# Kernel tuning notes

Measured on AMD Instinct MI355X. Metric: run time of the kernel, lower is better.

Reference implementation:

```python
import jax, jax.numpy as jnp
import numpy as np
import math

B, S, D = 2, 2048, 1024
H = 16
HD = D // H
FFN = 2048
E = 8
TOP_K = 2
CAP_FACTOR = 1.25
EPS = 1e-6
BASE = 10000.0
CAP = max(math.ceil(B * S * TOP_K * CAP_FACTOR / E), 1)  # 1280


def setup_inputs() -> dict:
    key = jax.random.key(0)
    ks = jax.random.split(key, 6)
    sd = 0.02
    return {
        "x": jax.random.normal(ks[0], (B, S, D), jnp.float32),
        "g1": jnp.ones((D,), jnp.float32),
        "w_qkv": jax.random.normal(ks[1], (D, 3 * D), jnp.float32) * sd,
        "w_o": jax.random.normal(ks[2], (D, D), jnp.float32) * sd,
        "g2": jnp.ones((D,), jnp.float32),
        "w_router": jax.random.normal(ks[3], (D, E), jnp.float32) * sd,
        "w1": jax.random.normal(ks[4], (E, D, FFN), jnp.float32) * sd,
        "w2": jax.random.normal(ks[5], (E, FFN, D), jnp.float32) * sd,
    }


def _rmsnorm(x, w):
    rms = jax.lax.rsqrt(jnp.mean(x * x, axis=-1, keepdims=True) + EPS)
    return w * x * rms


def _rope(x, cos, sin):
    # x: [b,h,s,hd]; consecutive pairs (2i, 2i+1) form complex numbers
    xr = x[..., 0::2]
    xi = x[..., 1::2]
    c = cos[None, None]  # [1,1,s,hd/2]
    s_ = sin[None, None]
    out_r = xr * c - xi * s_
    out_i = xr * s_ + xi * c
    return jnp.stack([out_r, out_i], axis=-1).reshape(x.shape)


def _mha(x, w_qkv, w_o):
    b, s, d = x.shape
    qkv = x @ w_qkv
    q, k, v = jnp.split(qkv, 3, axis=-1)
    to_heads = lambda z: z.reshape(b, s, H, HD).transpose(0, 2, 1, 3)
    q, k, v = to_heads(q), to_heads(k), to_heads(v)
    # rotary embedding
    theta = BASE ** (-2.0 * (jnp.arange(HD // 2, dtype=jnp.float32) / HD))
    freqs = jnp.arange(s, dtype=jnp.float32)[:, None] * theta[None, :]  # [s,hd/2]
    cos, sin = jnp.cos(freqs), jnp.sin(freqs)
    q = _rope(q, cos, sin)
    k = _rope(k, cos, sin)
    scores = jnp.einsum('bhqd,bhkd->bhqk', q, k) / jnp.sqrt(jnp.float32(HD))
    causal = jnp.tril(jnp.ones((s, s), dtype=bool))
    scores = jnp.where(causal, scores, -jnp.inf)
    attn = jax.nn.softmax(scores, axis=-1)
    y = jnp.einsum('bhqk,bhkd->bhqd', attn, v)
    y = y.transpose(0, 2, 1, 3).reshape(b, s, d)
    return y @ w_o


def _moe(x, w_router, w1, w2):
    b, s, d = x.shape
    t = b * s
    xf = x.reshape(t, d)
    logits = xf.astype(jnp.float32) @ w_router.astype(jnp.float32)
    probs = jax.nn.softmax(logits, axis=-1)  # [t,E]
    g, eidx = jax.lax.top_k(probs, TOP_K)  # [t,K]
    fg = g.reshape(t * TOP_K)
    fe = eidx.reshape(t * TOP_K)
    tok_of = jnp.arange(t * TOP_K) // TOP_K
    # per-expert masked gates, then capacity-based top-CAP selection
    masked = jnp.where(fe[None, :] == jnp.arange(E)[:, None], fg[None, :], -jnp.inf)  # [E, t*K]
    vals, idx = jax.lax.top_k(masked, CAP)  # [E, CAP]
    valid = jnp.isfinite(vals)
    gates = jnp.where(valid, vals, 0.0)  # dropped/empty slots get zero gate
    tok = tok_of[idx]  # [E, CAP] token ids (arbitrary for invalid slots, gate 0)
    xe = xf[tok]  # [E, CAP, d]
    h = jax.nn.relu(jnp.einsum('ecd,edf->ecf', xe, w1))
    ye = jnp.einsum('ecf,efd->ecd', h, w2) * gates[..., None]
    y = jnp.zeros_like(xf).at[tok.reshape(-1)].add(ye.reshape(-1, d))
    return y.reshape(b, s, d)


def reference(x, g1, w_qkv, w_o, g2, w_router, w1, w2):
    x = x + _mha(_rmsnorm(x, g1), w_qkv, w_o)
    x = x + _moe(_rmsnorm(x, g2), w_router, w1, w2)
    return x
```

## Files before the change

### kernel.cpp

```cpp
#include <hip/hip_runtime.h>
#include <math.h>


#define B_   2
#define S_   2048
#define D_   1024
#define H_   16
#define HD_  64
#define FFN_ 2048
#define E_   8
#define CAP_ 1280
#define T_   (B_*S_)

typedef unsigned short u16;
typedef __attribute__((ext_vector_type(8))) short     short8;
typedef __attribute__((ext_vector_type(8))) _Float16  half8;
typedef __attribute__((ext_vector_type(4))) _Float16  half4;
typedef __attribute__((ext_vector_type(8))) unsigned short ushort8v;
typedef __attribute__((ext_vector_type(4))) float     f32x4;

__device__ __forceinline__ u16 f2bf(float f) {
  unsigned u = __float_as_uint(f);
  return (u16)((u + 0x7fffu + ((u >> 16) & 1u)) >> 16);
}
__device__ __forceinline__ float bf2f(u16 h) {
  return __uint_as_float(((unsigned)h) << 16);
}
__device__ __forceinline__ u16 f2h(float f) {
  _Float16 h = (_Float16)f;
  return __builtin_bit_cast(u16, h);
}
__device__ __forceinline__ float h2f(u16 b) {
  return (float)__builtin_bit_cast(_Float16, b);
}

__device__ __forceinline__ void cstore(float* p, float v) { *p = v; }
__device__ __forceinline__ void cstore(u16* p, float v)   { *p = f2bf(v); }

__device__ __forceinline__ void glds16(const u16* g, u16* l) {
  __builtin_amdgcn_global_load_lds(
      (const __attribute__((address_space(1))) unsigned int*)g,
      (__attribute__((address_space(3))) unsigned int*)l, 16, 0, 0);
}

__global__ void init_k(int* cnt) {
  if (threadIdx.x < 16) cnt[threadIdx.x] = 0;
}

__global__ __launch_bounds__(256) void rmsnorm_k(const float* __restrict__ x,
                                                 const float* __restrict__ g,
                                                 float* __restrict__ of,
                                                 u16*   __restrict__ ob,
                                                 u16*   __restrict__ ohh,
                                                 u16*   __restrict__ ohl) {
  const int t = blockIdx.x, tid = threadIdx.x;
  const float4 xv = ((const float4*)(x + (size_t)t * D_))[tid];
  float ss = xv.x*xv.x + xv.y*xv.y + xv.z*xv.z + xv.w*xv.w;
  #pragma unroll
  for (int off = 32; off; off >>= 1) ss += __shfl_down(ss, off);
  __shared__ float wsum[4];
  if ((tid & 63) == 0) wsum[tid >> 6] = ss;
  __syncthreads();
  const float tot = wsum[0] + wsum[1] + wsum[2] + wsum[3];
  const float rms = 1.0f / sqrtf(tot * (1.0f / D_) + 1e-6f);
  const float4 gv = ((const float4*)g)[tid];
  float4 o;
  o.x = gv.x * xv.x * rms;
  o.y = gv.y * xv.y * rms;
  o.z = gv.z * xv.z * rms;
  o.w = gv.w * xv.w * rms;
  if (of) ((float4*)(of + (size_t)t * D_))[tid] = o;
  if (ob) {
    ushort4 h;
    h.x = f2bf(o.x); h.y = f2bf(o.y); h.z = f2bf(o.z); h.w = f2bf(o.w);
    ((ushort4*)(ob + (size_t)t * D_))[tid] = h;
  }
  if (ohh) {
    ushort4 hh, hl;
    hh.x = f2h(o.x); hl.x = f2h(o.x - h2f(hh.x));
    hh.y = f2h(o.y); hl.y = f2h(o.y - h2f(hh.y));
    hh.z = f2h(o.z); hl.z = f2h(o.z - h2f(hh.z));
    hh.w = f2h(o.w); hl.w = f2h(o.w - h2f(hh.w));
    ((ushort4*)(ohh + (size_t)t * D_))[tid] = hh;
    ((ushort4*)(ohl + (size_t)t * D_))[tid] = hl;
  }
}

template<bool RESID>
__global__ __launch_bounds__(256) void gemm_split(const u16* __restrict__ Ah,
                                                  const u16* __restrict__ Al,
                                                  const u16* __restrict__ Bh,
                                                  const u16* __restrict__ Bl,
                                                  const float* __restrict__ resid,
                                                  float* __restrict__ C,
                                                  int K, int lda, int ldb, int ldc) {
  __shared__ u16 AsH[128 * 32], AsL[128 * 32];
  __shared__ u16 BsH[128 * 32], BsL[128 * 32];
  const int tid = threadIdx.x;
  const int bm = blockIdx.y, bn = blockIdx.x;
  const int lane = tid & 63, wave = tid >> 6;
  const int wy = wave >> 1, wx = wave & 1;
  const int l15 = lane & 15, lq = lane >> 4;
  f32x4 acc[4][4];
  #pragma unroll
  for (int i = 0; i < 4; ++i)
    #pragma unroll
    for (int j = 0; j < 4; ++j)
      #pragma unroll
      for (int r = 0; r < 4; ++r) acc[i][j][r] = 0.0f;
  const int srow = lane >> 2, skc = (lane & 3) * 8;
  size_t ga[2], gb[2];
  int ldsoff[2];
  #pragma unroll
  for (int c = 0; c < 2; ++c) {
    const int q = wave * 2 + c;
    ga[c] = (size_t)(bm * 128 + q * 16 + srow) * lda + skc;
    gb[c] = (size_t)(bn * 128 + q * 16 + srow) * ldb + skc;
    ldsoff[c] = q * 512 + lane * 8;
  }

  for (int kt = 0; kt < K; kt += 32) {
    __syncthreads();
    #pragma unroll
    for (int c = 0; c < 2; ++c) {
      glds16(Ah + ga[c] + kt, &AsH[ldsoff[c]]);
      glds16(Al + ga[c] + kt, &AsL[ldsoff[c]]);
      glds16(Bh + gb[c] + kt, &BsH[ldsoff[c]]);
      glds16(Bl + gb[c] + kt, &BsL[ldsoff[c]]);
    }
    __syncthreads();
    half8 ah[4], al[4], bh[4], bl[4];
    #pragma unroll
    for (int i = 0; i < 4; ++i) {
      const int row = (wy * 64 + i * 16 + l15) * 32 + lq * 8;
      ah[i] = *(const half8*)&AsH[row];
      al[i] = *(const half8*)&AsL[row];
    }
    #pragma unroll
    for (int j = 0; j < 4; ++j) {
      const int row = (wx * 64 + j * 16 + l15) * 32 + lq * 8;
      bh[j] = *(const half8*)&BsH[row];
      bl[j] = *(const half8*)&BsL[row];
    }
    #pragma unroll
    for (int i = 0; i < 4; ++i)
      #pragma unroll
      for (int j = 0; j < 4; ++j) {
        acc[i][j] = __builtin_amdgcn_mfma_f32_16x16x32_f16(ah[i], bh[j], acc[i][j], 0, 0, 0);
        acc[i][j] = __builtin_amdgcn_mfma_f32_16x16x32_f16(ah[i], bl[j], acc[i][j], 0, 0, 0);
        acc[i][j] = __builtin_amdgcn_mfma_f32_16x16x32_f16(al[i], bh[j], acc[i][j], 0, 0, 0);
      }
  }
  #pragma unroll
  for (int i = 0; i < 4; ++i)
    #pragma unroll
    for (int j = 0; j < 4; ++j)
      #pragma unroll
      for (int r = 0; r < 4; ++r) {
        const int row = bm * 128 + wy * 64 + i * 16 + lq * 4 + r;
        const int col = bn * 128 + wx * 64 + j * 16 + l15;
        float v = acc[i][j][r];
        if (RESID) v += resid[(size_t)row * ldc + col];
        C[(size_t)row * ldc + col] = v;
      }
}

__global__ __launch_bounds__(256) void wsplit_t_k(const float* __restrict__ src,
                                                  u16* __restrict__ dh,
                                                  u16* __restrict__ dl,
                                                  int R, int C) {
  __shared__ float tile[32][33];
  const int tid = threadIdx.x;
  const int r0 = blockIdx.y * 32, c0 = blockIdx.x * 32;
  const int tx = tid & 31, ty = tid >> 5;
  #pragma unroll
  for (int i = 0; i < 4; ++i)
    tile[ty + i * 8][tx] = src[(size_t)(r0 + ty + i * 8) * C + c0 + tx];
  __syncthreads();
  #pragma unroll
  for (int i = 0; i < 4; ++i) {
    const float v = tile[tx][ty + i * 8];
    const u16 hh = f2h(v);
    const size_t o = (size_t)(c0 + ty + i * 8) * R + r0 + tx;
    dh[o] = hh;
    dl[o] = f2h(v - h2f(hh));
  }
}

__global__ __launch_bounds__(256) void ropesplit_k(const float* __restrict__ qkv,
                                                   u16* __restrict__ qhi, u16* __restrict__ qlo,
                                                   u16* __restrict__ khi, u16* __restrict__ klo) {
  const int i = blockIdx.x * 256 + threadIdx.x;
  const int j = i & 31;
  const int h = (i >> 5) & 15;
  const int t = i >> 9;
  const int s = t & (S_ - 1);
  const int b = t >> 11;
  const int bh = b * 16 + h;
  const float theta = (float)pow(10000.0, -(double)j / 32.0);
  const float fr = (float)s * theta;
  const float c = cosf(fr), sn = sinf(fr);
  const float2 q = *(const float2*)(qkv + (size_t)t * 3072 + h * 64 + 2 * j);
  const float2 k = *(const float2*)(qkv + (size_t)t * 3072 + 1024 + h * 64 + 2 * j);
  const float q0 = (q.x * c - q.y * sn) * 0.125f;
  const float q1 = (q.x * sn + q.y * c) * 0.125f;
  const float k0 = k.x * c - k.y * sn;
  const float k1 = k.x * sn + k.y * c;
  const size_t o = ((size_t)bh * S_ + s) * 32 + j;
  const u16 qh0 = f2bf(q0), qh1 = f2bf(q1);
  const u16 kh0 = f2bf(k0), kh1 = f2bf(k1);
  ((unsigned*)qhi)[o] = (unsigned)qh0 | ((unsigned)qh1 << 16);
  ((unsigned*)khi)[o] = (unsigned)kh0 | ((unsigned)kh1 << 16);
  const u16 ql0 = f2bf(q0 - bf2f(qh0)), ql1 = f2bf(q1 - bf2f(qh1));
  const u16 kl0 = f2bf(k0 - bf2f(kh0)), kl1 = f2bf(k1 - bf2f(kh1));
  ((unsigned*)qlo)[o] = (unsigned)ql0 | ((unsigned)ql1 << 16);
  ((unsigned*)klo)[o] = (unsigned)kl0 | ((unsigned)kl1 << 16);
}

__global__ __launch_bounds__(256) void vpack_k(const float* __restrict__ qkv,
                                               u16* __restrict__ vpk) {
  const int kt = blockIdx.x, bh = blockIdx.y;
  const int b = bh >> 4, h = bh & 15;
  const int tid = threadIdx.x;
  u16* dst = vpk + (size_t)(bh * 32 + kt) * 8192;
  #pragma unroll
  for (int i = 0; i < 4; ++i) {
    const int g = i * 256 + tid;
    const int lane = g & 63, n = (g >> 6) & 3, kc = g >> 8;
    const int lq = lane >> 4, l15 = lane & 15;
    const int key = kt * 64 + kc * 16 + lq * 4;
    const int d = n * 16 + l15;
    u16 out[8];
    #pragma unroll
    for (int j = 0; j < 4; ++j) {
      const float v = qkv[(size_t)(b * S_ + key + j) * 3072 + 2048 + h * 64 + d];
      const u16 hh = f2h(v);
      out[j] = hh;
      out[4 + j] = f2h(v - h2f(hh));
    }
    *(ushort8v*)(dst + g * 8) = *(ushort8v*)out;
  }
}

__global__ __launch_bounds__(256) void attn_mfma_k(const u16* __restrict__ qhi,
                                                   const u16* __restrict__ qlo,
                                                   const u16* __restrict__ khi,
                                                   const u16* __restrict__ klo,
                                                   const u16* __restrict__ vpk,
                                                   u16* __restrict__ ahh,
                                                   u16* __restrict__ ahl,
                                                   float* __restrict__ PO,
                                                   float* __restrict__ Pm,
                                                   float* __restrict__ Pl2) {
  __shared__ u16 Kh[64 * 68], Kl[64 * 68];
  __shared__ u16 Vp[8192];
  const int tid = threadIdx.x, lane = tid & 63, wave = tid >> 6;
  const int bi = blockIdx.x;
  int qt, k0, k1, chunk;
  bool partial;
  if (bi < 32) {
    qt = 31 - (bi >> 1); chunk = bi & 1;
    const int nk = qt + 1, cut = nk >> 1;
    k0 = chunk ? cut : 0;
    k1 = chunk ? nk : cut;
    partial = true;
  } else {
    qt = 47 - bi; chunk = 0; k0 = 0; k1 = qt + 1; partial = false;
  }
  const int bh = blockIdx.y;
  const int l15 = lane & 15, lq = lane >> 4;
  const size_t hb = (size_t)bh * S_ * 64;
  const int qrow = qt * 64 + wave * 16 + l15;
  short8 qh[2], ql[2];
  qh[0] = *(const short8*)(qhi + hb + (size_t)qrow * 64 + lq * 8);
  qh[1] = *(const short8*)(qhi + hb + (size_t)qrow * 64 + 32 + lq * 8);
  ql[0] = *(const short8*)(qlo + hb + (size_t)qrow * 64 + lq * 8);
  ql[1] = *(const short8*)(qlo + hb + (size_t)qrow * 64 + 32 + lq * 8);
  f32x4 O[4];
  #pragma unroll
  for (int n = 0; n < 4; ++n)
    #pragma unroll
    for (int r = 0; r < 4; ++r) O[n][r] = 0.0f;
  float m_i = -__builtin_inff(), l_i = 0.0f;

  for (int kt = k0; kt < k1; ++kt) {
    __syncthreads();
    {
      const u16* vg = vpk + (size_t)(bh * 32 + kt) * 8192 + wave * 2048;
      #pragma unroll
      for (int c = 0; c < 4; ++c)
        glds16(vg + c * 512 + lane * 8, &Vp[wave * 2048 + c * 512 + lane * 8]);
    }
    #pragma unroll
    for (int it = 0; it < 2; ++it) {
      const int idx = it * 256 + tid;
      const int row = idx >> 3, c8 = (idx & 7) * 8;
      const size_t koff = hb + (size_t)(kt * 64 + row) * 64 + c8;
      *(ushort8v*)&Kh[row * 68 + c8] = *(const ushort8v*)(khi + koff);
      *(ushort8v*)&Kl[row * 68 + c8] = *(const ushort8v*)(klo + koff);
    }
    __syncthreads();
    f32x4 sc[4];
    #pragma unroll
    for (int kc = 0; kc < 4; ++kc)
      #pragma unroll
      for (int r = 0; r < 4; ++r) sc[kc][r] = 0.0f;
    #pragma unroll
    for (int kc = 0; kc < 4; ++kc) {
      const int krow = (kc * 16 + l15) * 68 + lq * 8;
      const short8 kb0 = *(const short8*)&Kh[krow];
      const short8 kb1 = *(const short8*)&Kh[krow + 32];
      const short8 kl0 = *(const short8*)&Kl[krow];
      const short8 kl1 = *(const short8*)&Kl[krow + 32];
      sc[kc] = __builtin_amdgcn_mfma_f32_16x16x32_bf16(kb0, qh[0], sc[kc], 0, 0, 0);
      sc[kc] = __builtin_amdgcn_mfma_f32_16x16x32_bf16(kb1, qh[1], sc[kc], 0, 0, 0);
      sc[kc] = __builtin_amdgcn_mfma_f32_16x16x32_bf16(kb0, ql[0], sc[kc], 0, 0, 0);
      sc[kc] = __builtin_amdgcn_mfma_f32_16x16x32_bf16(kb1, ql[1], sc[kc], 0, 0, 0);
      sc[kc] = __builtin_amdgcn_mfma_f32_16x16x32_bf16(kl0, qh[0], sc[kc], 0, 0, 0);
      sc[kc] = __builtin_amdgcn_mfma_f32_16x16x32_bf16(kl1, qh[1], sc[kc], 0, 0, 0);
    }
    if (kt == qt) {
      #pragma unroll
      for (int kc = 0; kc < 4; ++kc)
        #pragma unroll
        for (int r = 0; r < 4; ++r)
          if (kc * 16 + lq * 4 + r > wave * 16 + l15) sc[kc][r] = -__builtin_inff();
    }
    float mx = -__builtin_inff();
    #pragma unroll
    for (int kc = 0; kc < 4; ++kc)
      #pragma unroll
      for (int r = 0; r < 4; ++r) mx = fmaxf(mx, sc[kc][r]);
    mx = fmaxf(mx, __shfl_xor(mx, 16));
    mx = fmaxf(mx, __shfl_xor(mx, 32));
    const float mn = fmaxf(m_i, mx);
    const float alpha = __expf(m_i - mn);
    m_i = mn;
    f32x4 p[4];
    float rs = 0.0f;
    #pragma unroll
    for (int kc = 0; kc < 4; ++kc)
      #pragma unroll
      for (int r = 0; r < 4; ++r) { p[kc][r] = __expf(sc[kc][r] - m_i); rs += p[kc][r]; }
    rs += __shfl_xor(rs, 16);
    rs += __shfl_xor(rs, 32);
    l_i = l_i * alpha + rs;
    #pragma unroll
    for (int r = 0; r < 4; ++r) {
      const float alr = __shfl(alpha, lq * 4 + r);
      #pragma unroll
      for (int n = 0; n < 4; ++n) O[n][r] *= alr;
    }
    half4 ph[4], pl[4];
    #pragma unroll
    for (int kc = 0; kc < 4; ++kc)
      #pragma unroll
      for (int r = 0; r < 4; ++r) {
        const _Float16 hi = (_Float16)p[kc][r];
        ph[kc][r] = hi;
        pl[kc][r] = (_Float16)(p[kc][r] - (float)hi);
      }
    #pragma unroll
    for (int n = 0; n < 4; ++n)
      #pragma unroll
      for (int kc = 0; kc < 4; ++kc) {
        const int g = ((kc * 4 + n) * 64 + lane) * 8;
        const half4 vh = *(const half4*)&Vp[g];
        const half4 vl = *(const half4*)&Vp[g + 4];
        O[n] = __builtin_amdgcn_mfma_f32_16x16x16f16(ph[kc], vh, O[n], 0, 0, 0);
        O[n] = __builtin_amdgcn_mfma_f32_16x16x16f16(ph[kc], vl, O[n], 0, 0, 0);
        O[n] = __builtin_amdgcn_mfma_f32_16x16x16f16(pl[kc], vh, O[n], 0, 0, 0);
      }
  }
  const int b = bh >> 4, h = bh & 15;
  if (!partial) {
    #pragma unroll
    for (int r = 0; r < 4; ++r) {
      const float lr = __shfl(l_i, lq * 4 + r);
      const float inv = 1.0f / lr;
      const int row = qt * 64 + wave * 16 + lq * 4 + r;
      const size_t base = (size_t)(b * S_ + row) * D_ + h * 64 + l15;
      #pragma unroll
      for (int n = 0; n < 4; ++n) {
        const float o = O[n][r] * inv;
        const u16 hh = f2h(o);
        ahh[base + n * 16] = hh;
        ahl[base + n * 16] = f2h(o - h2f(hh));
      }
    }
  } else {
    #pragma unroll
    for (int r = 0; r < 4; ++r) {
      const int prow = qt * 64 + wave * 16 + lq * 4 + r - 1024;
      const size_t idx = (size_t)(chunk * 32 + bh) * 1024 + prow;
      float* po = PO + idx * 64;
      #pragma unroll
      for (int n = 0; n < 4; ++n) po[n * 16 + l15] = O[n][r];
    }
    if (lq == 0) {
      const int prow = qt * 64 + wave * 16 + l15 - 1024;
      const size_t idx = (size_t)(chunk * 32 + bh) * 1024 + prow;
      Pm[idx] = m_i; Pl2[idx] = l_i;
    }
  }
}

__global__ __launch_bounds__(256) void attn_combine_k(const float* __restrict__ PO,
                                                      const float* __restrict__ Pm,
                                                      const float* __restrict__ Pl2,
                                                      u16* __restrict__ ahh,
                                                      u16* __restrict__ ahl) {
  const int tid = threadIdx.x;
  const int bh = blockIdx.y, b = bh >> 4, h = bh & 15;
  const int prow = blockIdx.x * 64 + (tid >> 2);
  const int d0 = (tid & 3) * 16;
  const size_t i0 = (size_t)bh * 1024 + prow;
  const size_t i1 = (size_t)(32 + bh) * 1024 + prow;
  const float m0 = Pm[i0], m1 = Pm[i1];
  const float M = fmaxf(m0, m1);
  const float w0 = __expf(m0 - M), w1 = __expf(m1 - M);
  const float inv = 1.0f / (w0 * Pl2[i0] + w1 * Pl2[i1]);
  const int row = 1024 + prow;
  const size_t ob = (size_t)(b * S_ + row) * D_ + h * 64 + d0;
  #pragma unroll
  for (int q4 = 0; q4 < 4; ++q4) {
    const float4 o0 = *(const float4*)(PO + i0 * 64 + d0 + q4 * 4);
    const float4 o1 = *(const float4*)(PO + i1 * 64 + d0 + q4 * 4);
    float v[4];
    v[0] = (w0 * o0.x + w1 * o1.x) * inv;
    v[1] = (w0 * o0.y + w1 * o1.y) * inv;
    v[2] = (w0 * o0.z + w1 * o1.z) * inv;
    v[3] = (w0 * o0.w + w1 * o1.w) * inv;
    ushort4 hh, hl;
    u16* ph = (u16*)&hh;
    u16* pl = (u16*)&hl;
    #pragma unroll
    for (int z = 0; z < 4; ++z) {
      ph[z] = f2h(v[z]);
      pl[z] = f2h(v[z] - h2f(ph[z]));
    }
    *(ushort4*)(ahh + ob + q4 * 4) = hh;
    *(ushort4*)(ahl + ob + q4 * 4) = hl;
  }
}

__global__ __launch_bounds__(256) void router_k(const float* __restrict__ y2,
                                                const float* __restrict__ wr,
                                                int*   __restrict__ cnt,
                                                int*   __restrict__ tok_e,
                                                float* __restrict__ tok_g,
                                                int*   __restrict__ tok_p,
                                                int*   __restrict__ etok) {
  const int wave = threadIdx.x >> 6, lane = threadIdx.x & 63;
  const int t = blockIdx.x * 4 + wave;
  const float* xr = y2 + (size_t)t * D_;
  float acc[8];
  #pragma unroll
  for (int e = 0; e < 8; ++e) acc[e] = 0.0f;
  for (int c = 0; c < 16; ++c) {
    const float xv = xr[c * 64 + lane];
    const float* w = wr + (size_t)(c * 64 + lane) * 8;
    #pragma unroll
    for (int e = 0; e < 8; ++e) acc[e] = fmaf(xv, w[e], acc[e]);
  }
  #pragma unroll
  for (int off = 32; off; off >>= 1)
    #pragma unroll
    for (int e = 0; e < 8; ++e) acc[e] += __shfl_down(acc[e], off);
  if (lane == 0) {
    float mx = acc[0];
    #pragma unroll
    for (int e = 1; e < 8; ++e) mx = fmaxf(mx, acc[e]);
    float ex[8], sum = 0.0f;
    #pragma unroll
    for (int e = 0; e < 8; ++e) { ex[e] = expf(acc[e] - mx); sum += ex[e]; }
    int e1 = 0;
    #pragma unroll
    for (int e = 1; e < 8; ++e) if (acc[e] > acc[e1]) e1 = e;
    int e2 = (e1 == 0) ? 1 : 0;
    #pragma unroll
    for (int e = 0; e < 8; ++e) if (e != e1 && acc[e] > acc[e2]) e2 = e;
    const float g1v = ex[e1] / sum, g2v = ex[e2] / sum;
    int p1 = atomicAdd(&cnt[e1], 1);
    int p2 = atomicAdd(&cnt[e2], 1);
    if (p1 < CAP_) etok[e1 * CAP_ + p1] = t; else p1 = -1;
    if (p2 < CAP_) etok[e2 * CAP_ + p2] = t; else p2 = -1;
    tok_e[2*t] = e1;   tok_e[2*t+1] = e2;
    tok_g[2*t] = g1v;  tok_g[2*t+1] = g2v;
    tok_p[2*t] = p1;   tok_p[2*t+1] = p2;
  }
}

__global__ __launch_bounds__(256) void gather_k(const u16* __restrict__ y2b,
                                                const int* __restrict__ etok,
                                                const int* __restrict__ cnt,
                                                u16* __restrict__ xe) {
  const int e = blockIdx.y, pos = blockIdx.x, tid = threadIdx.x;
  const int n = min(cnt[e], CAP_);
  ushort4* dst = (ushort4*)(xe + (size_t)(e * CAP_ + pos) * D_) + tid;
  if (pos < n) {
    const int t = etok[e * CAP_ + pos];
    *dst = ((const ushort4*)(y2b + (size_t)t * D_))[tid];
  } else {
    *dst = make_ushort4(0, 0, 0, 0);
  }
}

template<typename OT, bool RELU>
__global__ __launch_bounds__(256) void gemm_bt(const u16* __restrict__ A,
                                               const u16* __restrict__ Bt,
                                               OT* __restrict__ C,
                                               int M, int N, int K,
                                               int lda, int ldb, int ldc,
                                               long sAz, long sBz, long sCz) {
  __shared__ u16 As[128 * 32];
  __shared__ u16 Bs[128 * 32];
  const int tid = threadIdx.x;
  A  += (size_t)blockIdx.z * sAz;
  Bt += (size_t)blockIdx.z * sBz;
  C  += (size_t)blockIdx.z * sCz;
  const int bm = blockIdx.y, bn = blockIdx.x;
  const int lane = tid & 63, wave = tid >> 6;
  const int wy = wave >> 1, wx = wave & 1;
  const int l15 = lane & 15, lq = lane >> 4;
  f32x4 acc[4][4];
  #pragma unroll
  for (int i = 0; i < 4; ++i)
    #pragma unroll
    for (int j = 0; j < 4; ++j)
      #pragma unroll
      for (int r = 0; r < 4; ++r) acc[i][j][r] = 0.0f;
  const int srow = lane >> 2, skc = (lane & 3) * 8;
  size_t ga[2], gb[2];
  int ldsoff[2];
  #pragma unroll
  for (int c = 0; c < 2; ++c) {
    const int q = wave * 2 + c;
    ga[c] = (size_t)(bm * 128 + q * 16 + srow) * lda + skc;
    gb[c] = (size_t)(bn * 128 + q * 16 + srow) * ldb + skc;
    ldsoff[c] = q * 512 + lane * 8;
  }

  for (int kt = 0; kt < K; kt += 32) {
    __syncthreads();
    #pragma unroll
    for (int c = 0; c < 2; ++c) {
      glds16(A  + ga[c] + kt, &As[ldsoff[c]]);
      glds16(Bt + gb[c] + kt, &Bs[ldsoff[c]]);
    }
    __syncthreads();
    short8 a[4], b[4];
    #pragma unroll
    for (int i = 0; i < 4; ++i)
      a[i] = *(const short8*)&As[(wy * 64 + i * 16 + l15) * 32 + lq * 8];
    #pragma unroll
    for (int j = 0; j < 4; ++j)
      b[j] = *(const short8*)&Bs[(wx * 64 + j * 16 + l15) * 32 + lq * 8];
    #pragma unroll
    for (int i = 0; i < 4; ++i)
      #pragma unroll
      for (int j = 0; j < 4; ++j)
        acc[i][j] = __builtin_amdgcn_mfma_f32_16x16x32_bf16(a[i], b[j], acc[i][j], 0, 0, 0);
  }
  #pragma unroll
  for (int i = 0; i < 4; ++i)
    #pragma unroll
    for (int j = 0; j < 4; ++j)
      #pragma unroll
      for (int r = 0; r < 4; ++r) {
        const int row = bm * 128 + wy * 64 + i * 16 + lq * 4 + r;
        const int col = bn * 128 + wx * 64 + j * 16 + l15;
        float v = acc[i][j][r];
        if (RELU) v = fmaxf(v, 0.0f);
        cstore(C + (size_t)row * ldc + col, v);
      }
}

__global__ __launch_bounds__(256) void transpose_bf_k(const float* __restrict__ src,
                                                      u16* __restrict__ dst,
                                                      int R, int C) {
  __shared__ float tile[32][33];
  const int tid = threadIdx.x;
  const size_t zoff = (size_t)blockIdx.z * R * C;
  const int r0 = blockIdx.y * 32, c0 = blockIdx.x * 32;
  const int tx = tid & 31, ty = tid >> 5;
  #pragma unroll
  for (int i = 0; i < 4; ++i)
    tile[ty + i * 8][tx] = src[zoff + (size_t)(r0 + ty + i * 8) * C + c0 + tx];
  __syncthreads();
  #pragma unroll
  for (int i = 0; i < 4; ++i)
    dst[zoff + (size_t)(c0 + ty + i * 8) * R + r0 + tx] = f2bf(tile[tx][ty + i * 8]);
}

__global__ __launch_bounds__(256) void combine_k(const float* __restrict__ x2,
                                                 const float* __restrict__ ye,
                                                 const int*   __restrict__ tok_e,
                                                 const float* __restrict__ tok_g,
                                                 const int*   __restrict__ tok_p,
                                                 float* __restrict__ out) {
  const int t = blockIdx.x, tid = threadIdx.x;
  float4 v = ((const float4*)(x2 + (size_t)t * D_))[tid];
  #pragma unroll
  for (int r = 0; r < 2; ++r) {
    const int p = tok_p[2 * t + r];
    if (p >= 0) {
      const int e = tok_e[2 * t + r];
      const float g = tok_g[2 * t + r];
      const float4 y = ((const float4*)(ye + (size_t)(e * CAP_ + p) * D_))[tid];
      v.x = fmaf(g, y.x, v.x);
      v.y = fmaf(g, y.y, v.y);
      v.z = fmaf(g, y.z, v.z);
      v.w = fmaf(g, y.w, v.w);
    }
  }
  ((float4*)(out + (size_t)t * D_))[tid] = v;
}

extern "C" void kernel_launch(void* const* d_in, const int* in_sizes, int n_in,
                              void* d_out, int out_size, void* d_ws, size_t ws_size,
                              hipStream_t stream) {
  const float* x    = (const float*)d_in[0];
  const float* g1   = (const float*)d_in[1];
  const float* wqkv = (const float*)d_in[2];
  const float* wo   = (const float*)d_in[3];
  const float* g2   = (const float*)d_in[4];
  const float* wr   = (const float*)d_in[5];
  const float* w1   = (const float*)d_in[6];
  const float* w2   = (const float*)d_in[7];
  float* out = (float*)d_out;
  char* ws = (char*)d_ws;
  const size_t MB = 1ull << 20;

  u16*   y1hh  = (u16*)  (ws + 0);
  u16*   y1hl  = (u16*)  (ws + 8 * MB);
  u16*   ahh   = (u16*)  (ws + 16 * MB);
  u16*   ahl   = (u16*)  (ws + 24 * MB);
  u16*   hbf   = (u16*)  (ws + 0);
  float* qkv   = (float*)(ws + 40 * MB);
  float* PO    = (float*)(ws + 40 * MB);
  float* Pm    = (float*)(ws + 58 * MB);
  float* Pl2   = (float*)(ws + 59 * MB);
  u16*   xe    = (u16*)  (ws + 40 * MB);
  float* x2    = (float*)(ws + 88 * MB);
  float* y2    = (float*)(ws + 104 * MB);
  u16*   y2b   = (u16*)  (ws + 120 * MB);
  u16*   w1t   = (u16*)  (ws + 128 * MB);
  u16*   w2t   = (u16*)  (ws + 160 * MB);
  float* ye    = (float*)(ws + 192 * MB);
  u16*   wqh   = (u16*)  (ws + 192 * MB);
  u16*   wql   = (u16*)  (ws + 198 * MB);
  u16*   khi   = (u16*)  (ws + 192 * MB);
  u16*   klo   = (u16*)  (ws + 200 * MB);
  u16*   vpk   = (u16*)  (ws + 208 * MB);
  u16*   woh   = (u16*)  (ws + 224 * MB);
  u16*   wol   = (u16*)  (ws + 226 * MB);
  int*   cnt   = (int*)  (ws + 232 * MB);
  int*   tok_e = cnt + 16;
  float* tok_g = (float*)(tok_e + 2 * T_);
  int*   tok_p = (int*)  (tok_g + 2 * T_);
  int*   etok  = tok_p + 2 * T_;

  init_k<<<1, 64, 0, stream>>>(cnt);
  transpose_bf_k<<<dim3(FFN_/32, D_/32, E_), 256, 0, stream>>>(w1, w1t, D_, FFN_);
  transpose_bf_k<<<dim3(D_/32, FFN_/32, E_), 256, 0, stream>>>(w2, w2t, FFN_, D_);
  wsplit_t_k<<<dim3(3*D_/32, D_/32), 256, 0, stream>>>(wqkv, wqh, wql, D_, 3*D_);
  wsplit_t_k<<<dim3(D_/32, D_/32), 256, 0, stream>>>(wo, woh, wol, D_, D_);

  rmsnorm_k<<<T_, 256, 0, stream>>>(x, g1, (float*)nullptr, (u16*)nullptr, y1hh, y1hl);
  gemm_split<false><<<dim3(3 * D_ / 128, T_ / 128), 256, 0, stream>>>(
      y1hh, y1hl, wqh, wql, nullptr, qkv, D_, D_, D_, 3 * D_);
  ropesplit_k<<<T_ * H_ * 32 / 256, 256, 0, stream>>>(qkv, y1hh, y1hl, khi, klo);
  vpack_k<<<dim3(S_ / 64, B_ * H_), 256, 0, stream>>>(qkv, vpk);
  attn_mfma_k<<<dim3(48, B_ * H_), 256, 0, stream>>>(
      y1hh, y1hl, khi, klo, vpk, ahh, ahl, PO, Pm, Pl2);
  attn_combine_k<<<dim3(16, B_ * H_), 256, 0, stream>>>(PO, Pm, Pl2, ahh, ahl);
  gemm_split<true><<<dim3(D_ / 128, T_ / 128), 256, 0, stream>>>(
      ahh, ahl, woh, wol, x, x2, D_, D_, D_, D_);
  rmsnorm_k<<<T_, 256, 0, stream>>>(x2, g2, y2, y2b, (u16*)nullptr, (u16*)nullptr);
  router_k<<<T_ / 4, 256, 0, stream>>>(y2, wr, cnt, tok_e, tok_g, tok_p, etok);
  gather_k<<<dim3(CAP_, E_), 256, 0, stream>>>(y2b, etok, cnt, xe);
  gemm_bt<u16, true><<<dim3(FFN_/128, CAP_/128, E_), 256, 0, stream>>>(
      xe, w1t, hbf, CAP_, FFN_, D_, D_, D_, FFN_,
      (long)CAP_ * D_, (long)FFN_ * D_, (long)CAP_ * FFN_);
  gemm_bt<float, false><<<dim3(D_/128, CAP_/128, E_), 256, 0, stream>>>(
      hbf, w2t, ye, CAP_, D_, FFN_, FFN_, FFN_, D_,
      (long)CAP_ * FFN_, (long)D_ * FFN_, (long)CAP_ * D_);
  combine_k<<<T_, 256, 0, stream>>>(x2, ye, tok_e, tok_g, tok_p, out);
}
```

Measured before the change: 727.5 us.

## Prefetch next K/V tile into registers during attention compute

```diff
diff --git a/kernel.cpp b/kernel.cpp
--- a/kernel.cpp
+++ b/kernel.cpp
@@ -242,16 +242,16 @@
   }
 }
 
-__global__ __launch_bounds__(256) void attn_mfma_k(const u16* __restrict__ qhi,
-                                                   const u16* __restrict__ qlo,
-                                                   const u16* __restrict__ khi,
-                                                   const u16* __restrict__ klo,
-                                                   const u16* __restrict__ vpk,
-                                                   u16* __restrict__ ahh,
-                                                   u16* __restrict__ ahl,
-                                                   float* __restrict__ PO,
-                                                   float* __restrict__ Pm,
-                                                   float* __restrict__ Pl2) {
+__global__ __launch_bounds__(256, 4) void attn_mfma_k(const u16* __restrict__ qhi,
+                                                      const u16* __restrict__ qlo,
+                                                      const u16* __restrict__ khi,
+                                                      const u16* __restrict__ klo,
+                                                      const u16* __restrict__ vpk,
+                                                      u16* __restrict__ ahh,
+                                                      u16* __restrict__ ahl,
+                                                      float* __restrict__ PO,
+                                                      float* __restrict__ Pm,
+                                                      float* __restrict__ Pl2) {
   __shared__ u16 Kh[64 * 68], Kl[64 * 68];
   __shared__ u16 Vp[8192];
   const int tid = threadIdx.x, lane = tid & 63, wave = tid >> 6;
@@ -283,28 +283,46 @@
     for (int r = 0; r < 4; ++r) O[n][r] = 0.0f;
   float m_i = -__builtin_inff(), l_i = 0.0f;
 
+  const int sidx0 = tid,       srow0 = sidx0 >> 3, sc80 = (sidx0 & 7) * 8;
+  const int sidx1 = 256 + tid, srow1 = sidx1 >> 3, sc81 = (sidx1 & 7) * 8;
+  const int vlds = wave * 2048 + lane * 8;
+  ushort8v kregH[2], kregL[2], vreg[4];
+
+  auto issue_loads = [&](int kt) {
+    const size_t koff0 = hb + (size_t)(kt * 64 + srow0) * 64 + sc80;
+    const size_t koff1 = hb + (size_t)(kt * 64 + srow1) * 64 + sc81;
+    kregH[0] = *(const ushort8v*)(khi + koff0);
+    kregL[0] = *(const ushort8v*)(klo + koff0);
+    kregH[1] = *(const ushort8v*)(khi + koff1);
+    kregL[1] = *(const ushort8v*)(klo + koff1);
+    const u16* vg = vpk + (size_t)(bh * 32 + kt) * 8192 + vlds;
+    #pragma unroll
+    for (int c = 0; c < 4; ++c)
+      vreg[c] = *(const ushort8v*)(vg + c * 512);
+  };
+  auto write_lds = [&]() {
+    *(ushort8v*)&Kh[srow0 * 68 + sc80] = kregH[0];
+    *(ushort8v*)&Kl[srow0 * 68 + sc80] = kregL[0];
+    *(ushort8v*)&Kh[srow1 * 68 + sc81] = kregH[1];
+    *(ushort8v*)&Kl[srow1 * 68 + sc81] = kregL[1];
+    #pragma unroll
+    for (int c = 0; c < 4; ++c)
+      *(ushort8v*)&Vp[vlds + c * 512] = vreg[c];
+  };
+
+  issue_loads(k0);
+  write_lds();
+  __syncthreads();
+
   for (int kt = k0; kt < k1; ++kt) {
-    __syncthreads();
-    {
-      const u16* vg = vpk + (size_t)(bh * 32 + kt) * 8192 + wave * 2048;
-      #pragma unroll
-      for (int c = 0; c < 4; ++c)
-        glds16(vg + c * 512 + lane * 8, &Vp[wave * 2048 + c * 512 + lane * 8]);
-    }
-    #pragma unroll
-    for (int it = 0; it < 2; ++it) {
-      const int idx = it * 256 + tid;
-      const int row = idx >> 3, c8 = (idx & 7) * 8;
-      const size_t koff = hb + (size_t)(kt * 64 + row) * 64 + c8;
-      *(ushort8v*)&Kh[row * 68 + c8] = *(const ushort8v*)(khi + koff);
-      *(ushort8v*)&Kl[row * 68 + c8] = *(const ushort8v*)(klo + koff);
-    }
-    __syncthreads();
+    const bool pf = (kt + 1 < k1);
+    if (pf) issue_loads(kt + 1);
     f32x4 sc[4];
     #pragma unroll
     for (int kc = 0; kc < 4; ++kc)
       #pragma unroll
       for (int r = 0; r < 4; ++r) sc[kc][r] = 0.0f;
+    __builtin_amdgcn_s_setprio(1);
     #pragma unroll
     for (int kc = 0; kc < 4; ++kc) {
       const int krow = (kc * 16 + l15) * 68 + lq * 8;
@@ -319,6 +337,7 @@
       sc[kc] = __builtin_amdgcn_mfma_f32_16x16x32_bf16(kl0, qh[0], sc[kc], 0, 0, 0);
       sc[kc] = __builtin_amdgcn_mfma_f32_16x16x32_bf16(kl1, qh[1], sc[kc], 0, 0, 0);
     }
+    __builtin_amdgcn_s_setprio(0);
     if (kt == qt) {
       #pragma unroll
       for (int kc = 0; kc < 4; ++kc)
@@ -360,6 +379,7 @@
         ph[kc][r] = hi;
         pl[kc][r] = (_Float16)(p[kc][r] - (float)hi);
       }
+    __builtin_amdgcn_s_setprio(1);
     #pragma unroll
     for (int n = 0; n < 4; ++n)
       #pragma unroll
@@ -371,6 +391,10 @@
         O[n] = __builtin_amdgcn_mfma_f32_16x16x16f16(ph[kc], vl, O[n], 0, 0, 0);
         O[n] = __builtin_amdgcn_mfma_f32_16x16x16f16(pl[kc], vh, O[n], 0, 0, 0);
       }
+    __builtin_amdgcn_s_setprio(0);
+    __syncthreads();
+    if (pf) write_lds();
+    __syncthreads();
   }
   const int b = bh >> 4, h = bh & 15;
   if (!partial) {
```

After: 745.1 us. +2.4%, slower.
